# Kernel tuning notes

Measured on AMD Instinct MI355X. Metric: run time of the kernel, lower is better.

## Reference

```python
import jax, jax.numpy as jnp
import numpy as np

B, LAT, D = 64, 256, 64           # batch, latent dim, voxel grid side (== output image side)
ALPHA_ADJ = float(np.log2(D) + 2)  # alpha_adjust = log2(output_img_shape[0]) + 2


def _rotmat(a):
    """3x3 rotation matrix from Euler angles (x,y,z), R = Rz @ Ry @ Rx."""
    cx, sx = jnp.cos(a[0]), jnp.sin(a[0])
    cy, sy = jnp.cos(a[1]), jnp.sin(a[1])
    cz, sz = jnp.cos(a[2]), jnp.sin(a[2])
    Rx = jnp.array([[1, 0, 0], [0, 0, 0], [0, 0, 0]], jnp.float32).at[1, 1].set(cx).at[1, 2].set(-sx).at[2, 1].set(sx).at[2, 2].set(cx)
    Ry = jnp.array([[0, 0, 0], [0, 1, 0], [0, 0, 0]], jnp.float32).at[0, 0].set(cy).at[0, 2].set(sy).at[2, 0].set(-sy).at[2, 2].set(cy)
    Rz = jnp.array([[0, 0, 0], [0, 0, 0], [0, 0, 1]], jnp.float32).at[0, 0].set(cz).at[0, 1].set(-sz).at[1, 0].set(sz).at[1, 1].set(cz)
    return Rz @ Ry @ Rx


def _apply_transform(vol, R):
    """Rotate a [D,D,D] volume about its centre via trilinear sampling, zero padding."""
    d = vol.shape[0]
    c = (d - 1) / 2.0
    idx = jnp.arange(d, dtype=jnp.float32)
    gi, gj, gk = jnp.meshgrid(idx, idx, idx, indexing='ij')
    dst = jnp.stack([gi, gj, gk], axis=-1) - c        # [D,D,D,3]
    src = dst @ R.T + c                                # source coords
    x, y, z = src[..., 0], src[..., 1], src[..., 2]
    x0 = jnp.floor(x); y0 = jnp.floor(y); z0 = jnp.floor(z)
    fx, fy, fz = x - x0, y - y0, z - z0

    def gather(ix, iy, iz):
        valid = (ix >= 0) & (ix < d) & (iy >= 0) & (iy < d) & (iz >= 0) & (iz < d)
        ixc = jnp.clip(ix, 0, d - 1).astype(jnp.int32)
        iyc = jnp.clip(iy, 0, d - 1).astype(jnp.int32)
        izc = jnp.clip(iz, 0, d - 1).astype(jnp.int32)
        return jnp.where(valid, vol[ixc, iyc, izc], 0.0)

    c000 = gather(x0, y0, z0);     c001 = gather(x0, y0, z0 + 1)
    c010 = gather(x0, y0 + 1, z0); c011 = gather(x0, y0 + 1, z0 + 1)
    c100 = gather(x0 + 1, y0, z0); c101 = gather(x0 + 1, y0, z0 + 1)
    c110 = gather(x0 + 1, y0 + 1, z0); c111 = gather(x0 + 1, y0 + 1, z0 + 1)
    c00 = c000 * (1 - fz) + c001 * fz
    c01 = c010 * (1 - fz) + c011 * fz
    c10 = c100 * (1 - fz) + c101 * fz
    c11 = c110 * (1 - fz) + c111 * fz
    c0 = c00 * (1 - fy) + c01 * fy
    c1 = c10 * (1 - fy) + c11 * fy
    return c0 * (1 - fx) + c1 * fx


def setup_inputs() -> dict:
    key = jax.random.key(0)
    k1, k2, k3 = jax.random.split(key, 3)
    encoded = jax.random.normal(k1, (B, LAT), dtype=jnp.float32)
    W = jax.random.normal(k2, (LAT, D * D * D), dtype=jnp.float32) * 0.02
    b = jnp.zeros((D * D * D,), jnp.float32)
    angles = jax.random.uniform(k3, (B, 3), jnp.float32, -np.pi, np.pi)
    return {"encoded": encoded, "W": W, "b": b, "angles": angles}


def reference(encoded, W, b, angles):
    # voxel_generator: linear -> sigmoid -> [B, D, D, D], then alpha sharpening
    voxels = jax.nn.sigmoid(encoded @ W + b).reshape(B, D, D, D)
    voxels = voxels ** ALPHA_ADJ
    R = jax.vmap(_rotmat)(angles)                       # [B,3,3]
    views = jax.vmap(_apply_transform)(voxels, R)       # [B,D,D,D]
    # alpha compositing back-to-front along last (depth) axis
    alphas = jnp.moveaxis(views, -1, 0)[:, :, None]     # [Dz, B, 1, H, W]
    def step(img, a):
        return img * (1 - a) + a, None
    images, _ = jax.lax.scan(step, jnp.zeros((B, 1, D, D), jnp.float32), alphas, reverse=True)
    return 2 * images - 1
```

## Files before the change

### kernel.cpp

```cpp
#include <hip/hip_runtime.h>
#include <hip/hip_bf16.h>
#include <hip/hip_fp16.h>
#include <math.h>

#define BATCH 64
#define LAT   256
#define DVOX  64
#define VOX   (DVOX*DVOX*DVOX)

typedef __attribute__((ext_vector_type(8))) short short8;
typedef __attribute__((ext_vector_type(4))) float f32x4;
typedef unsigned uint32x4 __attribute__((ext_vector_type(4), aligned(4)));

__global__ void prep_kernel(const float* __restrict__ enc,
                            const float* __restrict__ angles,
                            unsigned short* __restrict__ encB,
                            float* __restrict__ Rmat) {
    int tid = threadIdx.x;
    for (int idx = tid; idx < BATCH * LAT; idx += blockDim.x) {
        __hip_bfloat16 h = __float2bfloat16(enc[idx]);
        encB[idx] = *reinterpret_cast<unsigned short*>(&h);
    }
    if (tid < BATCH) {
        float ax = angles[tid*3+0], ay = angles[tid*3+1], az = angles[tid*3+2];
        float cx = cosf(ax), sx = sinf(ax);
        float cy = cosf(ay), sy = sinf(ay);
        float cz = cosf(az), sz = sinf(az);
        float* R = Rmat + tid * 9;
        R[0] = cz*cy;  R[1] = cz*sy*sx - sz*cx;  R[2] = cz*sy*cx + sz*sx;
        R[3] = sz*cy;  R[4] = sz*sy*sx + cz*cx;  R[5] = sz*sy*cx - cz*sx;
        R[6] = -sy;    R[7] = cy*sx;             R[8] = cy*cx;
    }
}

__global__ __launch_bounds__(256, 2) void gemm_mfma_kernel(
        const unsigned short* __restrict__ encB,
        const float* __restrict__ W,
        const float* __restrict__ bias,
        __half* __restrict__ vox) {
    int wave = threadIdx.x >> 6;
    int lane = threadIdx.x & 63;
    int l15 = lane & 15, l4 = lane >> 4;
    int n4 = blockIdx.x * 256 + wave * 64 + 4 * l15;

    f32x4 acc[4][4];
#pragma unroll
    for (int t = 0; t < 4; ++t)
#pragma unroll
        for (int mt = 0; mt < 4; ++mt) acc[t][mt] = (f32x4){0.f, 0.f, 0.f, 0.f};

    const unsigned short* ap = encB + l15 * LAT + l4 * 8;
    const float* wp = W + (size_t)(l4 * 8) * VOX + n4;

    float4 w0[8], w1[8], w2[8];

    auto loadbuf = [&](float4* buf, int kb) {
        const float* q = wp + (size_t)kb * VOX;
#pragma unroll
        for (int j = 0; j < 8; ++j)
            buf[j] = *(const float4*)(q + (size_t)j * VOX);
    };

    auto consume = [&](const float4* w, int kb) {
        short8 a[4];
#pragma unroll
        for (int mt = 0; mt < 4; ++mt)
            a[mt] = *(const short8*)(ap + mt * 16 * LAT + kb);
        short8 bf[4];
#pragma unroll
        for (int t = 0; t < 4; ++t) {
            unsigned bw[4];
#pragma unroll
            for (int dw = 0; dw < 4; ++dw) {
                unsigned u0 = __float_as_uint(((const float*)&w[2 * dw])[t])     + 0x8000u;
                unsigned u1 = __float_as_uint(((const float*)&w[2 * dw + 1])[t]) + 0x8000u;
                bw[dw] = __builtin_amdgcn_perm(u1, u0, 0x07060302u);
            }
            bf[t] = *reinterpret_cast<short8*>(bw);
        }
#pragma unroll
        for (int t = 0; t < 4; ++t)
#pragma unroll
            for (int mt = 0; mt < 4; ++mt)
                acc[t][mt] = __builtin_amdgcn_mfma_f32_16x16x32_bf16(a[mt], bf[t], acc[t][mt], 0, 0, 0);
    };

    loadbuf(w0, 0);
    loadbuf(w1, 32);
    loadbuf(w2, 64);  consume(w0, 0);
    loadbuf(w0, 96);  consume(w1, 32);
    loadbuf(w1, 128); consume(w2, 64);
    loadbuf(w2, 160); consume(w0, 96);
    loadbuf(w0, 192); consume(w1, 128);
    loadbuf(w1, 224); consume(w2, 160);
    consume(w0, 192);
    consume(w1, 224);

    float4 bv = *(const float4*)(bias + n4);
#pragma unroll
    for (int mt = 0; mt < 4; ++mt) {
#pragma unroll
        for (int r = 0; r < 4; ++r) {
            int b = mt * 16 + l4 * 4 + r;
            float s[4];
#pragma unroll
            for (int t = 0; t < 4; ++t) {
                float x = acc[t][mt][r] + ((const float*)&bv)[t];
                float v = 1.f / (1.f + __expf(-x));
                v = v * v; v = v * v; v = v * v;
                s[t] = v;
            }
            __half2 h01 = __floats2half2_rn(s[0], s[1]);
            __half2 h23 = __floats2half2_rn(s[2], s[3]);
            uint2 pk;
            pk.x = *reinterpret_cast<unsigned*>(&h01);
            pk.y = *reinterpret_cast<unsigned*>(&h23);
            *reinterpret_cast<uint2*>(vox + (size_t)b * VOX + n4) = pk;
        }
    }
}

__device__ __forceinline__ float zlerp(unsigned e, float fz) {
    __half2 h = *reinterpret_cast<__half2*>(&e);
    float2 f = __half22float2(h);
    return f.x + (f.y - f.x) * fz;
}

__global__ __launch_bounds__(256) void render_lds_kernel(
        const __half* __restrict__ vox,
        const float* __restrict__ Rmat,
        float* __restrict__ out) {
    __shared__ unsigned sV[16 * 16 * 17];
    __shared__ float sT[4][64], sE[4][64];

    int bid  = blockIdx.x;
    int b    = bid & 63;
    int tile = bid >> 6;
    int t    = threadIdx.x;
    int pix  = t & 63, seg = t >> 6;
    int i0 = (tile >> 3) * 8, j0 = (tile & 7) * 8;
    int i = i0 + (pix >> 3);
    int j = j0 + (pix & 7);

    const float* Rb = Rmat + b * 9;
    float R0 = Rb[0], R1 = Rb[1], R2 = Rb[2];
    float R3 = Rb[3], R4 = Rb[4], R5 = Rb[5];
    float R6 = Rb[6], R7 = Rb[7], R8 = Rb[8];

    const float c = (DVOX - 1) * 0.5f;
    float di = (float)i - c, dj = (float)j - c;
    float xb = fmaf(R0, di, fmaf(R1, dj, c));
    float yb = fmaf(R3, di, fmaf(R4, dj, c));
    float zb = fmaf(R6, di, fmaf(R7, dj, c));

    float dic = (float)i0 + 3.5f - c;
    float djc = (float)j0 + 3.5f - c;
    float hwx = 3.5f * (fabsf(R0) + fabsf(R1) + fabsf(R2)) + 1e-3f;
    float hwy = 3.5f * (fabsf(R3) + fabsf(R4) + fabsf(R5)) + 1e-3f;
    float hwz = 3.5f * (fabsf(R6) + fabsf(R7) + fabsf(R8)) + 1e-3f;

    const unsigned short* V = (const unsigned short*)vox + (size_t)b * VOX;

    int rx = t >> 4, ry = t & 15;
    unsigned d[9];
    int xlo_n, ylo_n, zlo_n, s_n;

    auto bbox = [&](int ch) {
        float dkc = (float)(ch * 8) + 3.5f - c;
        float xc = fmaf(R0, dic, fmaf(R1, djc, fmaf(R2, dkc, c)));
        float yc = fmaf(R3, dic, fmaf(R4, djc, fmaf(R5, dkc, c)));
        float zc = fmaf(R6, dic, fmaf(R7, djc, fmaf(R8, dkc, c)));
        xlo_n = (int)floorf(xc - hwx);
        ylo_n = (int)floorf(yc - hwy);
        zlo_n = (int)floorf(zc - hwz);
        s_n   = zlo_n & ~1;
    };
    auto issue = [&]() {
        int gxc = min(max(xlo_n + rx, 0), DVOX - 1);
        int gyc = min(max(ylo_n + ry, 0), DVOX - 1);
        const unsigned* p = (const unsigned*)(V + ((gxc << 12) + (gyc << 6) + s_n));
        uint32x4 q0 = *(const uint32x4*)p;
        uint32x4 q1 = *(const uint32x4*)(p + 4);
        unsigned q2 = p[8];
        d[0] = q0[0]; d[1] = q0[1]; d[2] = q0[2]; d[3] = q0[3];
        d[4] = q1[0]; d[5] = q1[1]; d[6] = q1[2]; d[7] = q1[3];
        d[8] = q2;
    };

    bbox(7); issue();
    int xlo = xlo_n, ylo = ylo_n, zlo = zlo_n, s = s_n;

    float img = 0.f;
#pragma unroll 1
    for (int ch = 7; ch >= 0; --ch) {
        bool zint = (zlo >= 0) && (zlo + 17 <= DVOX);

        {
            bool rv = ((unsigned)(xlo + rx) < (unsigned)DVOX) &
                      ((unsigned)(ylo + ry) < (unsigned)DVOX);
            unsigned tt[9];
#pragma unroll
            for (int k = 0; k < 9; ++k) tt[k] = d[k];
            if (!zint) {
#pragma unroll
                for (int k = 0; k < 9; ++k) {
                    int h0 = s + 2 * k;
                    unsigned m = (((unsigned)h0 < (unsigned)DVOX) ? 0x0000FFFFu : 0u)
                               | (((unsigned)(h0 + 1) < (unsigned)DVOX) ? 0xFFFF0000u : 0u);
                    tt[k] &= m;
                }
            }
            unsigned rvm = rv ? 0xFFFFFFFFu : 0u;
#pragma unroll
            for (int k = 0; k < 9; ++k) tt[k] &= rvm;

            unsigned A[8];
#pragma unroll
            for (int m = 0; m < 8; ++m)
                A[m] = (tt[m] >> 16) | (tt[m + 1] << 16);

            unsigned* wrow = sV + t * 17;
            if (zlo & 1) {
#pragma unroll
                for (int m = 0; m < 8; ++m) {
                    wrow[2 * m]     = A[m];
                    wrow[2 * m + 1] = tt[m + 1];
                }
            } else {
#pragma unroll
                for (int m = 0; m < 8; ++m) {
                    wrow[2 * m]     = tt[m];
                    wrow[2 * m + 1] = A[m];
                }
            }
        }
        __syncthreads();

        if (ch > 0) { bbox(ch - 1); issue(); }

        float T = 1.f, E = 0.f;
        int k0 = ch * 8;
#pragma unroll
        for (int q = 1; q >= 0; --q) {
            int kk = 2 * seg + q;
            float dk = (float)(k0 + kk) - c;
            float x = fmaf(R2, dk, xb);
            float y = fmaf(R5, dk, yb);
            float z = fmaf(R8, dk, zb);

            float xf = floorf(x), yf = floorf(y), zf = floorf(z);
            float fx = x - xf, fy = y - yf, fz = z - zf;
            int xi = (int)xf - xlo;
            int yi = (int)yf - ylo;
            int zi = (int)zf - zlo;
            const unsigned* e = sV + (xi * 272 + yi * 17 + zi);

            float c00 = zlerp(e[0],   fz);
            float c01 = zlerp(e[17],  fz);
            float c10 = zlerp(e[272], fz);
            float c11 = zlerp(e[289], fz);
            float c0 = c00 + (c01 - c00) * fy;
            float c1 = c10 + (c11 - c10) * fy;
            float a  = c0  + (c1  - c0 ) * fx;

            E = E * (1.f - a) + a;
            T *= (1.f - a);
        }
        sT[seg][pix] = T;
        sE[seg][pix] = E;
        __syncthreads();

        if (seg == 0) {
            float im = img;
#pragma unroll
            for (int ss = 3; ss >= 0; --ss)
                im = fmaf(sT[ss][pix], im, sE[ss][pix]);
            img = im;
        }

        xlo = xlo_n; ylo = ylo_n; zlo = zlo_n; s = s_n;
    }

    if (seg == 0)
        out[b * (DVOX * DVOX) + i * DVOX + j] = 2.f * img - 1.f;
}

extern "C" void kernel_launch(void* const* d_in, const int* in_sizes, int n_in,
                              void* d_out, int out_size, void* d_ws, size_t ws_size,
                              hipStream_t stream) {
    const float* enc    = (const float*)d_in[0];
    const float* W      = (const float*)d_in[1];
    const float* bias   = (const float*)d_in[2];
    const float* angles = (const float*)d_in[3];
    float* out = (float*)d_out;

    char* ws = (char*)d_ws;
    unsigned short* encB = (unsigned short*)ws;
    float* Rmat          = (float*)(ws + 32768);
    __half* vox          = (__half*)(ws + 65536);

    prep_kernel<<<1, 256, 0, stream>>>(enc, angles, encB, Rmat);
    gemm_mfma_kernel<<<VOX / 256, 256, 0, stream>>>(encB, W, bias, vox);
    render_lds_kernel<<<BATCH * 64, 256, 0, stream>>>(vox, Rmat, out);
}
```

Baseline: 141.8 us.

## Fuse prep, GEMM and render into one persistent cooperative kernel

Replaces the three launches with a single cooperative kernel of 512 blocks. Each block converts the encodings to bf16 into LDS, computes two GEMM tiles, derives its rotation matrix, waits at a grid-wide sync, then renders eight tiles. This removes two kernel launches, their gaps and the separate prep pass. In exchange the grid-wide barrier serialises the phases, and the grid is capped at 512 blocks, fewer than the original render grid. If the cooperative launch fails, the old three-kernel path runs.

```diff
diff --git a/kernel.cpp b/kernel.cpp
--- a/kernel.cpp
+++ b/kernel.cpp
@@ -1,7 +1,10 @@
 #include <hip/hip_runtime.h>
+#include <hip/hip_cooperative_groups.h>
 #include <hip/hip_bf16.h>
 #include <hip/hip_fp16.h>
 #include <math.h>
+
+namespace cg = cooperative_groups;
 
 #define BATCH 64
 #define LAT   256
@@ -11,6 +14,270 @@
 typedef __attribute__((ext_vector_type(8))) short short8;
 typedef __attribute__((ext_vector_type(4))) float f32x4;
 typedef unsigned uint32x4 __attribute__((ext_vector_type(4), aligned(4)));
+
+#define EROW 264
+
+__device__ __forceinline__ float zlerp(unsigned e, float fz) {
+    __half2 h = *reinterpret_cast<__half2*>(&e);
+    float2 f = __half22float2(h);
+    return f.x + (f.y - f.x) * fz;
+}
+
+__global__ __launch_bounds__(256, 2) void fused_kernel(
+        const float* __restrict__ enc,
+        const float* __restrict__ W,
+        const float* __restrict__ bias,
+        const float* __restrict__ angles,
+        __half* __restrict__ vox,
+        float* __restrict__ out) {
+    __shared__ __align__(16) unsigned char smem[BATCH * EROW * 2];
+
+    int bid  = blockIdx.x;
+    int tid  = threadIdx.x;
+    int wave = tid >> 6, lane = tid & 63;
+    int l15  = lane & 15, l4 = lane >> 4;
+
+    unsigned short* eL = (unsigned short*)smem;
+    for (int idx = tid; idx < BATCH * LAT; idx += 256) {
+        int row = idx >> 8, k = idx & 255;
+        __hip_bfloat16 h = __float2bfloat16(enc[idx]);
+        eL[row * EROW + k] = *reinterpret_cast<unsigned short*>(&h);
+    }
+    __syncthreads();
+
+    const unsigned short* ap = eL + l15 * EROW + l4 * 8;
+
+#pragma unroll 1
+    for (int rep = 0; rep < 2; ++rep) {
+        int n0 = (bid + rep * 512) * 256;
+        int n4 = n0 + wave * 64 + 4 * l15;
+        const float* wp = W + (size_t)(l4 * 8) * VOX + n4;
+
+        f32x4 acc[4][4];
+#pragma unroll
+        for (int t = 0; t < 4; ++t)
+#pragma unroll
+            for (int mt = 0; mt < 4; ++mt) acc[t][mt] = (f32x4){0.f, 0.f, 0.f, 0.f};
+
+        float4 w0[8], w1[8], w2[8];
+        auto loadbuf = [&](float4* buf, int kb) {
+            const float* q = wp + (size_t)kb * VOX;
+#pragma unroll
+            for (int j = 0; j < 8; ++j)
+                buf[j] = *(const float4*)(q + (size_t)j * VOX);
+        };
+        auto consume = [&](const float4* w, int kb) {
+            short8 a[4];
+#pragma unroll
+            for (int mt = 0; mt < 4; ++mt)
+                a[mt] = *(const short8*)(ap + mt * 16 * EROW + kb);
+            short8 bf[4];
+#pragma unroll
+            for (int t = 0; t < 4; ++t) {
+                unsigned bw[4];
+#pragma unroll
+                for (int dw = 0; dw < 4; ++dw) {
+                    unsigned u0 = __float_as_uint(((const float*)&w[2 * dw])[t])     + 0x8000u;
+                    unsigned u1 = __float_as_uint(((const float*)&w[2 * dw + 1])[t]) + 0x8000u;
+                    bw[dw] = __builtin_amdgcn_perm(u1, u0, 0x07060302u);
+                }
+                bf[t] = *reinterpret_cast<short8*>(bw);
+            }
+#pragma unroll
+            for (int t = 0; t < 4; ++t)
+#pragma unroll
+                for (int mt = 0; mt < 4; ++mt)
+                    acc[t][mt] = __builtin_amdgcn_mfma_f32_16x16x32_bf16(a[mt], bf[t], acc[t][mt], 0, 0, 0);
+        };
+
+        loadbuf(w0, 0);
+        loadbuf(w1, 32);
+        loadbuf(w2, 64);  consume(w0, 0);
+        loadbuf(w0, 96);  consume(w1, 32);
+        loadbuf(w1, 128); consume(w2, 64);
+        loadbuf(w2, 160); consume(w0, 96);
+        loadbuf(w0, 192); consume(w1, 128);
+        loadbuf(w1, 224); consume(w2, 160);
+        consume(w0, 192);
+        consume(w1, 224);
+
+        float4 bv = *(const float4*)(bias + n4);
+#pragma unroll
+        for (int mt = 0; mt < 4; ++mt) {
+#pragma unroll
+            for (int r = 0; r < 4; ++r) {
+                int b = mt * 16 + l4 * 4 + r;
+                float s[4];
+#pragma unroll
+                for (int t = 0; t < 4; ++t) {
+                    float x = acc[t][mt][r] + ((const float*)&bv)[t];
+                    float v = 1.f / (1.f + __expf(-x));
+                    v = v * v; v = v * v; v = v * v;
+                    s[t] = v;
+                }
+                __half2 h01 = __floats2half2_rn(s[0], s[1]);
+                __half2 h23 = __floats2half2_rn(s[2], s[3]);
+                uint2 pk;
+                pk.x = *reinterpret_cast<unsigned*>(&h01);
+                pk.y = *reinterpret_cast<unsigned*>(&h23);
+                *reinterpret_cast<uint2*>(vox + (size_t)b * VOX + n4) = pk;
+            }
+        }
+    }
+
+    int b = bid & 63;
+    float ax = angles[b*3+0], ay = angles[b*3+1], az = angles[b*3+2];
+    float cx = cosf(ax), sx = sinf(ax);
+    float cy = cosf(ay), sy = sinf(ay);
+    float cz = cosf(az), sz = sinf(az);
+    float R0 = cz*cy, R1 = cz*sy*sx - sz*cx, R2 = cz*sy*cx + sz*sx;
+    float R3 = sz*cy, R4 = sz*sy*sx + cz*cx, R5 = sz*sy*cx - cz*sx;
+    float R6 = -sy,   R7 = cy*sx,            R8 = cy*cx;
+
+    cg::this_grid().sync();
+
+    unsigned* sV = (unsigned*)smem;
+    float (*sT)[64] = (float(*)[64])(smem + 17408);
+    float (*sE)[64] = (float(*)[64])(smem + 18432);
+
+    int pix = tid & 63, seg = tid >> 6;
+    int rx = tid >> 4, ry = tid & 15;
+    const float c = (DVOX - 1) * 0.5f;
+    float hwx = 3.5f * (fabsf(R0) + fabsf(R1) + fabsf(R2)) + 1e-3f;
+    float hwy = 3.5f * (fabsf(R3) + fabsf(R4) + fabsf(R5)) + 1e-3f;
+    float hwz = 3.5f * (fabsf(R6) + fabsf(R7) + fabsf(R8)) + 1e-3f;
+    const unsigned short* V = (const unsigned short*)vox + (size_t)b * VOX;
+
+#pragma unroll 1
+    for (int r = 0; r < 8; ++r) {
+        int tile = (bid + 512 * r) >> 6;
+        int i0 = (tile >> 3) * 8, j0 = (tile & 7) * 8;
+        int i = i0 + (pix >> 3);
+        int j = j0 + (pix & 7);
+
+        float di = (float)i - c, dj = (float)j - c;
+        float xb = fmaf(R0, di, fmaf(R1, dj, c));
+        float yb = fmaf(R3, di, fmaf(R4, dj, c));
+        float zb = fmaf(R6, di, fmaf(R7, dj, c));
+        float dic = (float)i0 + 3.5f - c;
+        float djc = (float)j0 + 3.5f - c;
+
+        unsigned d[9];
+        int xlo_n, ylo_n, zlo_n, s_n;
+        auto bbox = [&](int ch) {
+            float dkc = (float)(ch * 8) + 3.5f - c;
+            float xc = fmaf(R0, dic, fmaf(R1, djc, fmaf(R2, dkc, c)));
+            float yc = fmaf(R3, dic, fmaf(R4, djc, fmaf(R5, dkc, c)));
+            float zc = fmaf(R6, dic, fmaf(R7, djc, fmaf(R8, dkc, c)));
+            xlo_n = (int)floorf(xc - hwx);
+            ylo_n = (int)floorf(yc - hwy);
+            zlo_n = (int)floorf(zc - hwz);
+            s_n   = zlo_n & ~1;
+        };
+        auto issue = [&]() {
+            int gxc = min(max(xlo_n + rx, 0), DVOX - 1);
+            int gyc = min(max(ylo_n + ry, 0), DVOX - 1);
+            const unsigned* p = (const unsigned*)(V + ((gxc << 12) + (gyc << 6) + s_n));
+            uint32x4 q0 = *(const uint32x4*)p;
+            uint32x4 q1 = *(const uint32x4*)(p + 4);
+            unsigned q2 = p[8];
+            d[0] = q0[0]; d[1] = q0[1]; d[2] = q0[2]; d[3] = q0[3];
+            d[4] = q1[0]; d[5] = q1[1]; d[6] = q1[2]; d[7] = q1[3];
+            d[8] = q2;
+        };
+
+        bbox(7); issue();
+        int xlo = xlo_n, ylo = ylo_n, zlo = zlo_n, s = s_n;
+
+        float img = 0.f;
+#pragma unroll 1
+        for (int ch = 7; ch >= 0; --ch) {
+            bool zint = (zlo >= 0) && (zlo + 17 <= DVOX);
+            {
+                bool rv = ((unsigned)(xlo + rx) < (unsigned)DVOX) &
+                          ((unsigned)(ylo + ry) < (unsigned)DVOX);
+                unsigned tt[9];
+#pragma unroll
+                for (int k = 0; k < 9; ++k) tt[k] = d[k];
+                if (!zint) {
+#pragma unroll
+                    for (int k = 0; k < 9; ++k) {
+                        int h0 = s + 2 * k;
+                        unsigned m = (((unsigned)h0 < (unsigned)DVOX) ? 0x0000FFFFu : 0u)
+                                   | (((unsigned)(h0 + 1) < (unsigned)DVOX) ? 0xFFFF0000u : 0u);
+                        tt[k] &= m;
+                    }
+                }
+                unsigned rvm = rv ? 0xFFFFFFFFu : 0u;
+#pragma unroll
+                for (int k = 0; k < 9; ++k) tt[k] &= rvm;
+                unsigned A[8];
+#pragma unroll
+                for (int m = 0; m < 8; ++m)
+                    A[m] = (tt[m] >> 16) | (tt[m + 1] << 16);
+                unsigned* wrow = sV + tid * 17;
+                if (zlo & 1) {
+#pragma unroll
+                    for (int m = 0; m < 8; ++m) {
+                        wrow[2 * m]     = A[m];
+                        wrow[2 * m + 1] = tt[m + 1];
+                    }
+                } else {
+#pragma unroll
+                    for (int m = 0; m < 8; ++m) {
+                        wrow[2 * m]     = tt[m];
+                        wrow[2 * m + 1] = A[m];
+                    }
+                }
+            }
+            __syncthreads();
+
+            if (ch > 0) { bbox(ch - 1); issue(); }
+
+            float T = 1.f, E = 0.f;
+            int k0 = ch * 8;
+#pragma unroll
+            for (int q = 1; q >= 0; --q) {
+                int kk = 2 * seg + q;
+                float dk = (float)(k0 + kk) - c;
+                float x = fmaf(R2, dk, xb);
+                float y = fmaf(R5, dk, yb);
+                float z = fmaf(R8, dk, zb);
+                float xf = floorf(x), yf = floorf(y), zf = floorf(z);
+                float fx = x - xf, fy = y - yf, fz = z - zf;
+                int xi = (int)xf - xlo;
+                int yi = (int)yf - ylo;
+                int zi = (int)zf - zlo;
+                const unsigned* e = sV + (xi * 272 + yi * 17 + zi);
+                float c00 = zlerp(e[0],   fz);
+                float c01 = zlerp(e[17],  fz);
+                float c10 = zlerp(e[272], fz);
+                float c11 = zlerp(e[289], fz);
+                float c0 = c00 + (c01 - c00) * fy;
+                float c1 = c10 + (c11 - c10) * fy;
+                float a  = c0  + (c1  - c0 ) * fx;
+                E = E * (1.f - a) + a;
+                T *= (1.f - a);
+            }
+            sT[seg][pix] = T;
+            sE[seg][pix] = E;
+            __syncthreads();
+
+            if (seg == 0) {
+                float im = img;
+#pragma unroll
+                for (int ss = 3; ss >= 0; --ss)
+                    im = fmaf(sT[ss][pix], im, sE[ss][pix]);
+                img = im;
+            }
+            xlo = xlo_n; ylo = ylo_n; zlo = zlo_n; s = s_n;
+        }
+
+        if (seg == 0)
+            out[b * (DVOX * DVOX) + i * DVOX + j] = 2.f * img - 1.f;
+        __syncthreads();
+    }
+}
 
 __global__ void prep_kernel(const float* __restrict__ enc,
                             const float* __restrict__ angles,
@@ -33,7 +300,7 @@
     }
 }
 
-__global__ __launch_bounds__(256, 2) void gemm_mfma_kernel(
+__global__ __launch_bounds__(256, 2) void gemm_fb_kernel(
         const unsigned short* __restrict__ encB,
         const float* __restrict__ W,
         const float* __restrict__ bias,
@@ -51,16 +318,12 @@
 
     const unsigned short* ap = encB + l15 * LAT + l4 * 8;
     const float* wp = W + (size_t)(l4 * 8) * VOX + n4;
-
     float4 w0[8], w1[8], w2[8];
-
     auto loadbuf = [&](float4* buf, int kb) {
         const float* q = wp + (size_t)kb * VOX;
 #pragma unroll
-        for (int j = 0; j < 8; ++j)
-            buf[j] = *(const float4*)(q + (size_t)j * VOX);
+        for (int j = 0; j < 8; ++j) buf[j] = *(const float4*)(q + (size_t)j * VOX);
     };
-
     auto consume = [&](const float4* w, int kb) {
         short8 a[4];
 #pragma unroll
@@ -84,7 +347,6 @@
             for (int mt = 0; mt < 4; ++mt)
                 acc[t][mt] = __builtin_amdgcn_mfma_f32_16x16x32_bf16(a[mt], bf[t], acc[t][mt], 0, 0, 0);
     };
-
     loadbuf(w0, 0);
     loadbuf(w1, 32);
     loadbuf(w2, 64);  consume(w0, 0);
@@ -120,13 +382,7 @@
     }
 }
 
-__device__ __forceinline__ float zlerp(unsigned e, float fz) {
-    __half2 h = *reinterpret_cast<__half2*>(&e);
-    float2 f = __half22float2(h);
-    return f.x + (f.y - f.x) * fz;
-}
-
-__global__ __launch_bounds__(256) void render_lds_kernel(
+__global__ __launch_bounds__(256) void render_fb_kernel(
         const __half* __restrict__ vox,
         const float* __restrict__ Rmat,
         float* __restrict__ out) {
@@ -152,19 +408,16 @@
     float xb = fmaf(R0, di, fmaf(R1, dj, c));
     float yb = fmaf(R3, di, fmaf(R4, dj, c));
     float zb = fmaf(R6, di, fmaf(R7, dj, c));
-
     float dic = (float)i0 + 3.5f - c;
     float djc = (float)j0 + 3.5f - c;
     float hwx = 3.5f * (fabsf(R0) + fabsf(R1) + fabsf(R2)) + 1e-3f;
     float hwy = 3.5f * (fabsf(R3) + fabsf(R4) + fabsf(R5)) + 1e-3f;
     float hwz = 3.5f * (fabsf(R6) + fabsf(R7) + fabsf(R8)) + 1e-3f;
-
     const unsigned short* V = (const unsigned short*)vox + (size_t)b * VOX;
 
     int rx = t >> 4, ry = t & 15;
     unsigned d[9];
     int xlo_n, ylo_n, zlo_n, s_n;
-
     auto bbox = [&](int ch) {
         float dkc = (float)(ch * 8) + 3.5f - c;
         float xc = fmaf(R0, dic, fmaf(R1, djc, fmaf(R2, dkc, c)));
@@ -194,7 +447,6 @@
 #pragma unroll 1
     for (int ch = 7; ch >= 0; --ch) {
         bool zint = (zlo >= 0) && (zlo + 17 <= DVOX);
-
         {
             bool rv = ((unsigned)(xlo + rx) < (unsigned)DVOX) &
                       ((unsigned)(ylo + ry) < (unsigned)DVOX);
@@ -213,29 +465,20 @@
             unsigned rvm = rv ? 0xFFFFFFFFu : 0u;
 #pragma unroll
             for (int k = 0; k < 9; ++k) tt[k] &= rvm;
-
             unsigned A[8];
 #pragma unroll
             for (int m = 0; m < 8; ++m)
                 A[m] = (tt[m] >> 16) | (tt[m + 1] << 16);
-
             unsigned* wrow = sV + t * 17;
             if (zlo & 1) {
 #pragma unroll
-                for (int m = 0; m < 8; ++m) {
-                    wrow[2 * m]     = A[m];
-                    wrow[2 * m + 1] = tt[m + 1];
-                }
+                for (int m = 0; m < 8; ++m) { wrow[2*m] = A[m]; wrow[2*m+1] = tt[m+1]; }
             } else {
 #pragma unroll
-                for (int m = 0; m < 8; ++m) {
-                    wrow[2 * m]     = tt[m];
-                    wrow[2 * m + 1] = A[m];
-                }
+                for (int m = 0; m < 8; ++m) { wrow[2*m] = tt[m]; wrow[2*m+1] = A[m]; }
             }
         }
         __syncthreads();
-
         if (ch > 0) { bbox(ch - 1); issue(); }
 
         float T = 1.f, E = 0.f;
@@ -247,14 +490,12 @@
             float x = fmaf(R2, dk, xb);
             float y = fmaf(R5, dk, yb);
             float z = fmaf(R8, dk, zb);
-
             float xf = floorf(x), yf = floorf(y), zf = floorf(z);
             float fx = x - xf, fy = y - yf, fz = z - zf;
             int xi = (int)xf - xlo;
             int yi = (int)yf - ylo;
             int zi = (int)zf - zlo;
             const unsigned* e = sV + (xi * 272 + yi * 17 + zi);
-
             float c00 = zlerp(e[0],   fz);
             float c01 = zlerp(e[17],  fz);
             float c10 = zlerp(e[272], fz);
@@ -262,14 +503,12 @@
             float c0 = c00 + (c01 - c00) * fy;
             float c1 = c10 + (c11 - c10) * fy;
             float a  = c0  + (c1  - c0 ) * fx;
-
             E = E * (1.f - a) + a;
             T *= (1.f - a);
         }
         sT[seg][pix] = T;
         sE[seg][pix] = E;
         __syncthreads();
-
         if (seg == 0) {
             float im = img;
 #pragma unroll
@@ -277,7 +516,6 @@
                 im = fmaf(sT[ss][pix], im, sE[ss][pix]);
             img = im;
         }
-
         xlo = xlo_n; ylo = ylo_n; zlo = zlo_n; s = s_n;
     }
 
@@ -299,7 +537,13 @@
     float* Rmat          = (float*)(ws + 32768);
     __half* vox          = (__half*)(ws + 65536);
 
-    prep_kernel<<<1, 256, 0, stream>>>(enc, angles, encB, Rmat);
-    gemm_mfma_kernel<<<VOX / 256, 256, 0, stream>>>(encB, W, bias, vox);
-    render_lds_kernel<<<BATCH * 64, 256, 0, stream>>>(vox, Rmat, out);
+    void* args[] = {(void*)&enc, (void*)&W, (void*)&bias,
+                    (void*)&angles, (void*)&vox, (void*)&out};
+    hipError_t err = hipLaunchCooperativeKernel(
+        (const void*)fused_kernel, dim3(512), dim3(256), args, 0, stream);
+    if (err != hipSuccess) {
+        prep_kernel<<<1, 256, 0, stream>>>(enc, angles, encB, Rmat);
+        gemm_fb_kernel<<<VOX / 256, 256, 0, stream>>>(encB, W, bias, vox);
+        render_fb_kernel<<<BATCH * 64, 256, 0, stream>>>(vox, Rmat, out);
+    }
 }
```

After: 201.9 us. 42.3% more time.
